# Kernel tuning notes

Hardware: AMD Instinct MI355X
Metric: run time of the kernel (lower is better)

Reference implementation:

```python
import jax, jax.numpy as jnp
import numpy as np

E = 8           # num_local_experts
H = 1024        # hidden_size
F = 1024        # moe_ffn_hidden_size (per-half; fc1 out = 2*F due to GLU)
T = 16384       # total dispatched tokens
GLU_LINEAR_OFFSET = 1.0


def setup_inputs() -> dict:
    key = jax.random.key(0)
    ks = jax.random.split(key, 7)
    s1 = 1.0 / np.sqrt(H)
    s2 = 1.0 / np.sqrt(F)
    return {
        "hidden_states": jax.random.normal(ks[0], (T, H), jnp.float32),
        "tokens_per_expert": jnp.full((E,), T // E, dtype=jnp.int64),
        "probs": jax.random.uniform(ks[1], (T,), jnp.float32),
        # expert params; torch Linear W is [out,in], stored here as [in,out] (same math)
        "W1": jax.random.uniform(ks[2], (E, H, 2 * F), jnp.float32, -s1, s1),
        "b1": jax.random.uniform(ks[3], (E, 2 * F), jnp.float32, -s1, s1),
        "W2": jax.random.uniform(ks[4], (E, F, H), jnp.float32, -s2, s2),
        "b2": jax.random.uniform(ks[5], (E, H), jnp.float32, -s2, s2),
    }


def reference(hidden_states, tokens_per_expert, probs, W1, b1, W2, b2):
    # Tokens arrive grouped contiguously by expert with equal counts (as in
    # setup_inputs), so the split/loop/cat in the torch module is exactly a
    # reshape + grouped (batched) GEMM over the expert axis.
    e = W1.shape[0]
    t, h = hidden_states.shape
    x = hidden_states.reshape(e, t // e, h)            # [E, Tpe, H]
    p = probs.reshape(e, t // e)                       # [E, Tpe]
    # fc1 (gated)
    y = jnp.einsum('eth,ehf->etf', x, W1) + b1[:, None, :]  # [E, Tpe, 2F]
    gate, lin = jnp.split(y, 2, axis=-1)
    a = jax.nn.silu(gate) * (lin + GLU_LINEAR_OFFSET)       # [E, Tpe, F]
    a = a * p[..., None]                                    # per-token scale
    # fc2
    out = jnp.einsum('etf,efh->eth', a, W2) + b2[:, None, :]
    return out.reshape(t, h)
```

## Files before the change

### kernel.cpp

```cpp
#include <hip/hip_runtime.h>
#include <hip/hip_bf16.h>
#include <stdint.h>

#define T_TOK 16384
#define H_DIM 1024
#define F_DIM 1024
#define E_NUM 8
#define TPE   2048

typedef unsigned short u16;
typedef __attribute__((ext_vector_type(8))) short bf16x8;
typedef __attribute__((ext_vector_type(4))) float f32x4;
typedef __attribute__((ext_vector_type(8))) u16 u16x8;

__device__ __forceinline__ u16 f2bf(float x) {
  unsigned int u = __float_as_uint(x);
  u = (u + 0x7fffu + ((u >> 16) & 1u)) >> 16;
  return (u16)u;
}

#define GLD16(gp, lp)                                                          \
  __builtin_amdgcn_global_load_lds(                                            \
      (const __attribute__((address_space(1))) void*)(gp),                     \
      (__attribute__((address_space(3))) void*)(lp), 16, 0, 0)

__global__ __launch_bounds__(256) void prep(
    const float* __restrict__ x, const float* __restrict__ W1,
    const float* __restrict__ W2, u16* __restrict__ xbf,
    u16* __restrict__ w1t, u16* __restrict__ w2t) {
  __shared__ float tile[64][65];
  const int b = blockIdx.x;
  const int t = threadIdx.x;
  if (b < 2048) {
    const int n8 = (T_TOK * H_DIM) / 8;
    for (int i = b * 256 + t; i < n8; i += 2048 * 256) {
      const float4* s = (const float4*)(x + (size_t)i * 8);
      float4 a = s[0], c = s[1];
      u16x8 o;
      o[0] = f2bf(a.x); o[1] = f2bf(a.y); o[2] = f2bf(a.z); o[3] = f2bf(a.w);
      o[4] = f2bf(c.x); o[5] = f2bf(c.y); o[6] = f2bf(c.z); o[7] = f2bf(c.w);
      *(u16x8*)(xbf + (size_t)i * 8) = o;
    }
    return;
  }
  const float* src; u16* dst; int R, C, id;
  if (b < 6144) { src = W1; dst = w1t; R = H_DIM; C = 2 * F_DIM; id = b - 2048; }
  else          { src = W2; dst = w2t; R = F_DIM; C = H_DIM;     id = b - 6144; }
  int nCt = C >> 6, nRt = R >> 6;
  int per = nCt * nRt;
  int e = id / per;
  int r2 = id - e * per;
  int rt = r2 / nCt, ct = r2 - rt * nCt;
  const float* s = src + (size_t)e * R * C + (size_t)(rt << 6) * C + (ct << 6);
  int lr = t >> 4, lc = (t & 15) << 2;
#pragma unroll
  for (int i = 0; i < 4; i++) {
    float4 v = *(const float4*)(s + (size_t)(lr + i * 16) * C + lc);
    tile[lr + i * 16][lc + 0] = v.x;
    tile[lr + i * 16][lc + 1] = v.y;
    tile[lr + i * 16][lc + 2] = v.z;
    tile[lr + i * 16][lc + 3] = v.w;
  }
  __syncthreads();
  u16* d = dst + (size_t)e * C * R + (size_t)(ct << 6) * R + (rt << 6);
  int orow = t >> 2, ok = (t & 3) << 4;
  u16x8 o0, o1;
#pragma unroll
  for (int i = 0; i < 8; i++) o0[i] = f2bf(tile[ok + i][orow]);
#pragma unroll
  for (int i = 0; i < 8; i++) o1[i] = f2bf(tile[ok + 8 + i][orow]);
  *(u16x8*)(d + (size_t)orow * R + ok) = o0;
  *(u16x8*)(d + (size_t)orow * R + ok + 8) = o1;
}


#define DSA(b, mi)                                                             \
  _Pragma("unroll") for (int m2_ = 0; m2_ < 2; ++m2_)                          \
  _Pragma("unroll") for (int ks_ = 0; ks_ < 2; ++ks_)                          \
      aF[m2_][ks_] = *(const bf16x8*)(sm + (b) * 32768 + aRowBase +            \
                                      ((mi) * 2 + m2_) * 2048 + koff[ks_]);

#define DSB(b)                                                                 \
  _Pragma("unroll") for (int n_ = 0; n_ < 4; ++n_)                             \
  _Pragma("unroll") for (int ks_ = 0; ks_ < 2; ++ks_)                          \
      bF[n_][ks_] = *(const bf16x8*)(sm + 65536 + (b) * 32768 + bRowBase +     \
                                     n_ * 2048 + koff[ks_]);

#define MFMA16(mi)                                                             \
  _Pragma("unroll") for (int n_ = 0; n_ < 4; ++n_)                             \
  _Pragma("unroll") for (int m2_ = 0; m2_ < 2; ++m2_)                          \
  _Pragma("unroll") for (int ks_ = 0; ks_ < 2; ++ks_)                          \
      acc[(mi) * 2 + m2_][n_] = __builtin_amdgcn_mfma_f32_16x16x32_bf16(       \
          aF[m2_][ks_], bF[n_][ks_], acc[(mi) * 2 + m2_][n_], 0, 0, 0);

#define PF_A(db, q, d) GLD16(aP[q] + (d), sm + (db) * 32768 + (q) * 8192 + tid * 16)
#define PF_B(db, q, d) GLD16(bP[q] + (d), sm + 65536 + (db) * 32768 + (q) * 8192 + tid * 16)

#define PHASE(b, mi, PFC, WTC)                                                 \
  do {                                                                         \
    DSA(b, mi);                                                                \
    if ((mi) == 0) { DSB(b); }                                                 \
    PFC                                                                        \
    __builtin_amdgcn_s_setprio(1);                                             \
    MFMA16(mi);                                                                \
    __builtin_amdgcn_s_setprio(0);                                             \
    WTC                                                                        \
    __builtin_amdgcn_s_barrier();                                              \
  } while (0)

#define KLOOP_BODY                                                             \
         \
  PF_B(0, 0, 0); PF_B(0, 1, 0); PF_B(0, 2, 0); PF_B(0, 3, 0);                  \
  PF_A(0, 0, 0); PF_A(0, 1, 0); PF_A(0, 2, 0); PF_A(0, 3, 0);                  \
  PF_B(1, 0, 64); PF_B(1, 1, 64); PF_B(1, 2, 64); PF_B(1, 3, 64);              \
  asm volatile("s_waitcnt vmcnt(4)" ::: "memory");                             \
  __builtin_amdgcn_s_barrier();                                                \
  for (int it = 0; it < 7; ++it) {                                             \
    PHASE(0, 0, PF_A(1, 0, 64); PF_A(1, 1, 64);, );                            \
    PHASE(0, 1, PF_A(1, 2, 64); PF_A(1, 3, 64);, );                            \
    PHASE(0, 2, PF_B(0, 0, 128); PF_B(0, 1, 128);, );                          \
    PHASE(0, 3, PF_B(0, 2, 128); PF_B(0, 3, 128);,                             \
          asm volatile("s_waitcnt vmcnt(4)" ::: "memory"););                   \
    PHASE(1, 0, PF_A(0, 0, 128); PF_A(0, 1, 128);, );                          \
    PHASE(1, 1, PF_A(0, 2, 128); PF_A(0, 3, 128);, );                          \
    PHASE(1, 2, PF_B(1, 0, 192); PF_B(1, 1, 192);, );                          \
    PHASE(1, 3, PF_B(1, 2, 192); PF_B(1, 3, 192);,                             \
          asm volatile("s_waitcnt vmcnt(4)" ::: "memory"););                   \
    _Pragma("unroll") for (int q_ = 0; q_ < 4; ++q_) {                         \
      aP[q_] += 128; bP[q_] += 128;                                            \
    }                                                                          \
  }                                                                            \
                   \
  PHASE(0, 0, PF_A(1, 0, 64); PF_A(1, 1, 64);, );                              \
  PHASE(0, 1, PF_A(1, 2, 64); PF_A(1, 3, 64);, );                              \
  PHASE(0, 2, , );                                                             \
  PHASE(0, 3, , asm volatile("s_waitcnt vmcnt(0)" ::: "memory"););             \
  PHASE(1, 0, , );                                                             \
  PHASE(1, 1, , );                                                             \
  PHASE(1, 2, , );                                                             \
  PHASE(1, 3, , );

__global__ __launch_bounds__(512, 2) void gemm1_8p(
    const u16* __restrict__ xbf, const u16* __restrict__ w1t,
    const float* __restrict__ b1, const float* __restrict__ probs,
    u16* __restrict__ abf) {
  extern __shared__ char sm[];
  const int tid = threadIdx.x;
  const int lane = tid & 63;
  const int wid = tid >> 6;
  const int wm = wid >> 2, wn = wid & 3;
  const int bid = blockIdx.x;
  const int e = bid & 7;
  const int inner = bid >> 3;
  const int mt = inner >> 3, ct = inner & 7;
  const int tokBase = e * TPE + mt * 256;
  const int c0 = ct * 128;
  const int lrow = lane & 15, lkhi = lane >> 4;

  const u16* aP[4]; const u16* bP[4];
#pragma unroll
  for (int q = 0; q < 4; ++q) {
    int lin = q * 8192 + tid * 16;
    int lg = lin ^ (((lin >> 7) & 7) << 4);
    int row = lg >> 7, kk = (lg & 127) >> 1;
    aP[q] = xbf + (size_t)(tokBase + row) * H_DIM + kk;
    int col = (((row >> 5) & 1) << 10) + c0 + ((row >> 6) << 5) + (row & 31);
    bP[q] = w1t + (size_t)(e * 2 * F_DIM + col) * H_DIM + kk;
  }
  const int aRowBase = (wm * 128 + lrow) * 128;
  const int bRowBase = (wn * 64 + lrow) * 128;
  int koff[2];
#pragma unroll
  for (int ks = 0; ks < 2; ++ks)
    koff[ks] = ((ks << 6) | (lkhi << 4)) ^ ((lane & 7) << 4);

  f32x4 acc[8][4];
#pragma unroll
  for (int i = 0; i < 8; ++i)
#pragma unroll
    for (int j = 0; j < 4; ++j) acc[i][j] = f32x4{0.f, 0.f, 0.f, 0.f};
  bf16x8 aF[2][2], bF[4][2];

  KLOOP_BODY

#pragma unroll
  for (int j = 0; j < 2; ++j) {
    int cf = c0 + wn * 32 + j * 16 + lrow;
    float gb = b1[e * 2 * F_DIM + cf];
    float lb = b1[e * 2 * F_DIM + F_DIM + cf];
#pragma unroll
    for (int i = 0; i < 8; ++i) {
      int trow = tokBase + wm * 128 + i * 16 + lkhi * 4;
#pragma unroll
      for (int r = 0; r < 4; ++r) {
        float g = acc[i][j][r] + gb;
        float l = acc[i][j + 2][r] + lb + 1.0f;
        float p = probs[trow + r];
        float sig = 1.0f / (1.0f + __expf(-g));
        abf[(size_t)(trow + r) * F_DIM + cf] = f2bf(g * sig * l * p);
      }
    }
  }
}

__global__ __launch_bounds__(512, 2) void gemm2_8p(
    const u16* __restrict__ abf, const u16* __restrict__ w2t,
    const float* __restrict__ b2, float* __restrict__ out) {
  extern __shared__ char sm[];
  const int tid = threadIdx.x;
  const int lane = tid & 63;
  const int wid = tid >> 6;
  const int wm = wid >> 2, wn = wid & 3;
  const int bid = blockIdx.x;
  const int e = bid & 7;
  const int inner = bid >> 3;
  const int mt = inner >> 2, nt = inner & 3;
  const int tokBase = e * TPE + mt * 256;
  const int h0 = nt * 256;
  const int lrow = lane & 15, lkhi = lane >> 4;

  const u16* aP[4]; const u16* bP[4];
#pragma unroll
  for (int q = 0; q < 4; ++q) {
    int lin = q * 8192 + tid * 16;
    int lg = lin ^ (((lin >> 7) & 7) << 4);
    int row = lg >> 7, kk = (lg & 127) >> 1;
    aP[q] = abf + (size_t)(tokBase + row) * F_DIM + kk;
    bP[q] = w2t + (size_t)(e * H_DIM + h0 + row) * F_DIM + kk;
  }
  const int aRowBase = (wm * 128 + lrow) * 128;
  const int bRowBase = (wn * 64 + lrow) * 128;
  int koff[2];
#pragma unroll
  for (int ks = 0; ks < 2; ++ks)
    koff[ks] = ((ks << 6) | (lkhi << 4)) ^ ((lane & 7) << 4);

  f32x4 acc[8][4];
#pragma unroll
  for (int i = 0; i < 8; ++i)
#pragma unroll
    for (int j = 0; j < 4; ++j) acc[i][j] = f32x4{0.f, 0.f, 0.f, 0.f};
  bf16x8 aF[2][2], bF[4][2];

  KLOOP_BODY

#pragma unroll
  for (int j = 0; j < 4; ++j) {
    int h = h0 + wn * 64 + j * 16 + lrow;
    float bb = b2[e * H_DIM + h];
#pragma unroll
    for (int i = 0; i < 8; ++i) {
      int trow = tokBase + wm * 128 + i * 16 + lkhi * 4;
#pragma unroll
      for (int r = 0; r < 4; ++r)
        out[(size_t)(trow + r) * H_DIM + h] = acc[i][j][r] + bb;
    }
  }
}

extern "C" void kernel_launch(void* const* d_in, const int* in_sizes, int n_in,
                              void* d_out, int out_size, void* d_ws,
                              size_t ws_size, hipStream_t stream) {
  const float* x     = (const float*)d_in[0];
  const float* probs = (const float*)d_in[2];
  const float* W1    = (const float*)d_in[3];
  const float* b1    = (const float*)d_in[4];
  const float* W2    = (const float*)d_in[5];
  const float* b2    = (const float*)d_in[6];
  float* out = (float*)d_out;

  if (ws_size < 117440512u) return;
  char* ws = (char*)d_ws;
  u16* xbf = (u16*)(ws);
  u16* w1t = (u16*)(ws + 33554432);
  u16* w2t = (u16*)(ws + 67108864);
  u16* abf = (u16*)(ws + 83886080);

  (void)hipFuncSetAttribute(reinterpret_cast<const void*>(gemm1_8p),
                            hipFuncAttributeMaxDynamicSharedMemorySize, 131072);
  (void)hipFuncSetAttribute(reinterpret_cast<const void*>(gemm2_8p),
                            hipFuncAttributeMaxDynamicSharedMemorySize, 131072);

  prep<<<8192, 256, 0, stream>>>(x, W1, W2, xbf, w1t, w2t);
  gemm1_8p<<<E_NUM * 8 * 8, 512, 131072, stream>>>(xbf, w1t, b1, probs, abf);
  gemm2_8p<<<E_NUM * 8 * 4, 512, 131072, stream>>>(abf, w2t, b2, out);
}
```

Measured before the change: 151.5 us.

## Fuse fp32-to-bf16 activation conversion into gemm1 A-tile loading

Removes the separate pass that converts the fp32 hidden states to a bf16 workspace buffer. Gemm1 now loads fp32 A tiles into registers, converts them and writes them to LDS inside the pipelined K loop, while the weight transpose becomes two standalone kernels. This avoids writing and re-reading a 32MB intermediate, but doubles the A-operand global traffic per tile (re-read across the 8 column tiles), adds VGPR pressure and conversion ALU work in the hot loop, and changes the wait-count pipelining.

Result: slower. 169.6 us (+12.0%).

```diff
diff --git a/kernel.cpp b/kernel.cpp
--- a/kernel.cpp
+++ b/kernel.cpp
@@ -24,34 +24,17 @@
       (const __attribute__((address_space(1))) void*)(gp),                     \
       (__attribute__((address_space(3))) void*)(lp), 16, 0, 0)
 
-__global__ __launch_bounds__(256) void prep(
-    const float* __restrict__ x, const float* __restrict__ W1,
-    const float* __restrict__ W2, u16* __restrict__ xbf,
-    u16* __restrict__ w1t, u16* __restrict__ w2t) {
+__global__ __launch_bounds__(256) void transpose_cvt(
+    const float* __restrict__ src, u16* __restrict__ dst, int R, int C) {
   __shared__ float tile[64][65];
-  const int b = blockIdx.x;
-  const int t = threadIdx.x;
-  if (b < 2048) {
-    const int n8 = (T_TOK * H_DIM) / 8;
-    for (int i = b * 256 + t; i < n8; i += 2048 * 256) {
-      const float4* s = (const float4*)(x + (size_t)i * 8);
-      float4 a = s[0], c = s[1];
-      u16x8 o;
-      o[0] = f2bf(a.x); o[1] = f2bf(a.y); o[2] = f2bf(a.z); o[3] = f2bf(a.w);
-      o[4] = f2bf(c.x); o[5] = f2bf(c.y); o[6] = f2bf(c.z); o[7] = f2bf(c.w);
-      *(u16x8*)(xbf + (size_t)i * 8) = o;
-    }
-    return;
-  }
-  const float* src; u16* dst; int R, C, id;
-  if (b < 6144) { src = W1; dst = w1t; R = H_DIM; C = 2 * F_DIM; id = b - 2048; }
-  else          { src = W2; dst = w2t; R = F_DIM; C = H_DIM;     id = b - 6144; }
   int nCt = C >> 6, nRt = R >> 6;
   int per = nCt * nRt;
-  int e = id / per;
-  int r2 = id - e * per;
+  int b = blockIdx.x;
+  int e = b / per;
+  int r2 = b - e * per;
   int rt = r2 / nCt, ct = r2 - rt * nCt;
   const float* s = src + (size_t)e * R * C + (size_t)(rt << 6) * C + (ct << 6);
+  int t = threadIdx.x;
   int lr = t >> 4, lc = (t & 15) << 2;
 #pragma unroll
   for (int i = 0; i < 4; i++) {
@@ -96,8 +79,35 @@
 #define PF_A(db, q, d) GLD16(aP[q] + (d), sm + (db) * 32768 + (q) * 8192 + tid * 16)
 #define PF_B(db, q, d) GLD16(bP[q] + (d), sm + 65536 + (db) * 32768 + (q) * 8192 + tid * 16)
 
-#define PHASE(b, mi, PFC, WTC)                                                 \
+#define VMW(N) asm volatile("s_waitcnt vmcnt(" #N ")" ::: "memory");
+
+#define A_WAIT(N)                                                              \
+  asm volatile("s_waitcnt vmcnt(" #N ")" ::: "memory");                        \
+  __builtin_amdgcn_sched_barrier(0);
+
+#define A_ISSUE(OFFE)                                                          \
+  _Pragma("unroll") for (int q_ = 0; q_ < 4; ++q_) {                           \
+    const float* p_ = afp[q_] + (OFFE);                                        \
+    asm volatile("global_load_dwordx4 %0, %2, off\n\t"                         \
+                 "global_load_dwordx4 %1, %2, off offset:16"                   \
+                 : "=&v"(av[2 * q_]), "=&v"(av[2 * q_ + 1])                    \
+                 : "v"(p_));                                                   \
+  }
+
+#define A_CVTWRITE(db)                                                         \
+  _Pragma("unroll") for (int q_ = 0; q_ < 4; ++q_) {                           \
+    u16x8 w_;                                                                  \
+    _Pragma("unroll") for (int e_ = 0; e_ < 4; ++e_) {                         \
+      w_[e_] = f2bf(av[2 * q_][e_]);                                           \
+      w_[e_ + 4] = f2bf(av[2 * q_ + 1][e_]);                                   \
+    }                                                                          \
+    *(u16x8*)(sm + (db) * 32768 + q_ * 8192 + tid * 16) = w_;                  \
+  }                                                                            \
+  __builtin_amdgcn_sched_barrier(0);
+
+#define PHASE1(b, mi, PRE, PFC, WTC)                                           \
   do {                                                                         \
+    PRE                                                                        \
     DSA(b, mi);                                                                \
     if ((mi) == 0) { DSB(b); }                                                 \
     PFC                                                                        \
@@ -108,40 +118,8 @@
     __builtin_amdgcn_s_barrier();                                              \
   } while (0)
 
-#define KLOOP_BODY                                                             \
-         \
-  PF_B(0, 0, 0); PF_B(0, 1, 0); PF_B(0, 2, 0); PF_B(0, 3, 0);                  \
-  PF_A(0, 0, 0); PF_A(0, 1, 0); PF_A(0, 2, 0); PF_A(0, 3, 0);                  \
-  PF_B(1, 0, 64); PF_B(1, 1, 64); PF_B(1, 2, 64); PF_B(1, 3, 64);              \
-  asm volatile("s_waitcnt vmcnt(4)" ::: "memory");                             \
-  __builtin_amdgcn_s_barrier();                                                \
-  for (int it = 0; it < 7; ++it) {                                             \
-    PHASE(0, 0, PF_A(1, 0, 64); PF_A(1, 1, 64);, );                            \
-    PHASE(0, 1, PF_A(1, 2, 64); PF_A(1, 3, 64);, );                            \
-    PHASE(0, 2, PF_B(0, 0, 128); PF_B(0, 1, 128);, );                          \
-    PHASE(0, 3, PF_B(0, 2, 128); PF_B(0, 3, 128);,                             \
-          asm volatile("s_waitcnt vmcnt(4)" ::: "memory"););                   \
-    PHASE(1, 0, PF_A(0, 0, 128); PF_A(0, 1, 128);, );                          \
-    PHASE(1, 1, PF_A(0, 2, 128); PF_A(0, 3, 128);, );                          \
-    PHASE(1, 2, PF_B(1, 0, 192); PF_B(1, 1, 192);, );                          \
-    PHASE(1, 3, PF_B(1, 2, 192); PF_B(1, 3, 192);,                             \
-          asm volatile("s_waitcnt vmcnt(4)" ::: "memory"););                   \
-    _Pragma("unroll") for (int q_ = 0; q_ < 4; ++q_) {                         \
-      aP[q_] += 128; bP[q_] += 128;                                            \
-    }                                                                          \
-  }                                                                            \
-                   \
-  PHASE(0, 0, PF_A(1, 0, 64); PF_A(1, 1, 64);, );                              \
-  PHASE(0, 1, PF_A(1, 2, 64); PF_A(1, 3, 64);, );                              \
-  PHASE(0, 2, , );                                                             \
-  PHASE(0, 3, , asm volatile("s_waitcnt vmcnt(0)" ::: "memory"););             \
-  PHASE(1, 0, , );                                                             \
-  PHASE(1, 1, , );                                                             \
-  PHASE(1, 2, , );                                                             \
-  PHASE(1, 3, , );
-
 __global__ __launch_bounds__(512, 2) void gemm1_8p(
-    const u16* __restrict__ xbf, const u16* __restrict__ w1t,
+    const float* __restrict__ x, const u16* __restrict__ w1t,
     const float* __restrict__ b1, const float* __restrict__ probs,
     u16* __restrict__ abf) {
   extern __shared__ char sm[];
@@ -157,13 +135,14 @@
   const int c0 = ct * 128;
   const int lrow = lane & 15, lkhi = lane >> 4;
 
-  const u16* aP[4]; const u16* bP[4];
+  const float* afp[4];
+  const u16* bP[4];
 #pragma unroll
   for (int q = 0; q < 4; ++q) {
     int lin = q * 8192 + tid * 16;
     int lg = lin ^ (((lin >> 7) & 7) << 4);
     int row = lg >> 7, kk = (lg & 127) >> 1;
-    aP[q] = xbf + (size_t)(tokBase + row) * H_DIM + kk;
+    afp[q] = x + (size_t)(tokBase + row) * H_DIM + kk;
     int col = (((row >> 5) & 1) << 10) + c0 + ((row >> 6) << 5) + (row & 31);
     bP[q] = w1t + (size_t)(e * 2 * F_DIM + col) * H_DIM + kk;
   }
@@ -180,8 +159,37 @@
 #pragma unroll
     for (int j = 0; j < 4; ++j) acc[i][j] = f32x4{0.f, 0.f, 0.f, 0.f};
   bf16x8 aF[2][2], bF[4][2];
-
-  KLOOP_BODY
+  float4 av[8];
+
+  A_ISSUE(0);
+  PF_B(0, 0, 0); PF_B(0, 1, 0); PF_B(0, 2, 0); PF_B(0, 3, 0);
+  A_WAIT(4); A_CVTWRITE(0);
+  A_ISSUE(64);
+  PF_B(1, 0, 64); PF_B(1, 1, 64); PF_B(1, 2, 64); PF_B(1, 3, 64);
+  VMW(12)
+  asm volatile("s_waitcnt lgkmcnt(0)" ::: "memory");
+  __builtin_amdgcn_s_barrier();
+
+  for (int it = 0; it < 7; ++it) {
+    PHASE1(0, 0, A_WAIT(4) A_CVTWRITE(1) A_ISSUE(128), , );
+    PHASE1(0, 1, , , );
+    PHASE1(0, 2, , PF_B(0, 0, 128); PF_B(0, 1, 128);, );
+    PHASE1(0, 3, , PF_B(0, 2, 128); PF_B(0, 3, 128);, VMW(12));
+    PHASE1(1, 0, A_WAIT(4) A_CVTWRITE(0) A_ISSUE(192), , );
+    PHASE1(1, 1, , , );
+    PHASE1(1, 2, , PF_B(1, 0, 192); PF_B(1, 1, 192);, );
+    PHASE1(1, 3, , PF_B(1, 2, 192); PF_B(1, 3, 192);, VMW(12));
+#pragma unroll
+    for (int q_ = 0; q_ < 4; ++q_) { afp[q_] += 128; bP[q_] += 128; }
+  }
+  PHASE1(0, 0, A_WAIT(4) A_CVTWRITE(1), , );
+  PHASE1(0, 1, , , );
+  PHASE1(0, 2, , , );
+  PHASE1(0, 3, , , VMW(0));
+  PHASE1(1, 0, , , );
+  PHASE1(1, 1, , , );
+  PHASE1(1, 2, , , );
+  PHASE1(1, 3, , , );
 
 #pragma unroll
   for (int j = 0; j < 2; ++j) {
@@ -202,6 +210,18 @@
     }
   }
 }
+
+#define PHASE2(b, mi, PFC, WTC)                                                \
+  do {                                                                         \
+    DSA(b, mi);                                                                \
+    if ((mi) == 0) { DSB(b); }                                                 \
+    PFC                                                                        \
+    __builtin_amdgcn_s_setprio(1);                                             \
+    MFMA16(mi);                                                                \
+    __builtin_amdgcn_s_setprio(0);                                             \
+    WTC                                                                        \
+    __builtin_amdgcn_s_barrier();                                              \
+  } while (0)
 
 __global__ __launch_bounds__(512, 2) void gemm2_8p(
     const u16* __restrict__ abf, const u16* __restrict__ w2t,
@@ -242,7 +262,31 @@
     for (int j = 0; j < 4; ++j) acc[i][j] = f32x4{0.f, 0.f, 0.f, 0.f};
   bf16x8 aF[2][2], bF[4][2];
 
-  KLOOP_BODY
+  PF_B(0, 0, 0); PF_B(0, 1, 0); PF_B(0, 2, 0); PF_B(0, 3, 0);
+  PF_A(0, 0, 0); PF_A(0, 1, 0); PF_A(0, 2, 0); PF_A(0, 3, 0);
+  PF_B(1, 0, 64); PF_B(1, 1, 64); PF_B(1, 2, 64); PF_B(1, 3, 64);
+  VMW(4)
+  __builtin_amdgcn_s_barrier();
+  for (int it = 0; it < 7; ++it) {
+    PHASE2(0, 0, PF_A(1, 0, 64); PF_A(1, 1, 64);, );
+    PHASE2(0, 1, PF_A(1, 2, 64); PF_A(1, 3, 64);, );
+    PHASE2(0, 2, PF_B(0, 0, 128); PF_B(0, 1, 128);, );
+    PHASE2(0, 3, PF_B(0, 2, 128); PF_B(0, 3, 128);, VMW(4));
+    PHASE2(1, 0, PF_A(0, 0, 128); PF_A(0, 1, 128);, );
+    PHASE2(1, 1, PF_A(0, 2, 128); PF_A(0, 3, 128);, );
+    PHASE2(1, 2, PF_B(1, 0, 192); PF_B(1, 1, 192);, );
+    PHASE2(1, 3, PF_B(1, 2, 192); PF_B(1, 3, 192);, VMW(4));
+#pragma unroll
+    for (int q_ = 0; q_ < 4; ++q_) { aP[q_] += 128; bP[q_] += 128; }
+  }
+  PHASE2(0, 0, PF_A(1, 0, 64); PF_A(1, 1, 64);, );
+  PHASE2(0, 1, PF_A(1, 2, 64); PF_A(1, 3, 64);, );
+  PHASE2(0, 2, , );
+  PHASE2(0, 3, , VMW(0));
+  PHASE2(1, 0, , );
+  PHASE2(1, 1, , );
+  PHASE2(1, 2, , );
+  PHASE2(1, 3, , );
 
 #pragma unroll
   for (int j = 0; j < 4; ++j) {
@@ -269,19 +313,21 @@
   const float* b2    = (const float*)d_in[6];
   float* out = (float*)d_out;
 
-  if (ws_size < 117440512u) return;
+  if (ws_size < 83886080u) return;
   char* ws = (char*)d_ws;
-  u16* xbf = (u16*)(ws);
-  u16* w1t = (u16*)(ws + 33554432);
-  u16* w2t = (u16*)(ws + 67108864);
-  u16* abf = (u16*)(ws + 83886080);
+  u16* w1t = (u16*)(ws);
+  u16* w2t = (u16*)(ws + 33554432);
+  u16* abf = (u16*)(ws + 50331648);
 
   (void)hipFuncSetAttribute(reinterpret_cast<const void*>(gemm1_8p),
                             hipFuncAttributeMaxDynamicSharedMemorySize, 131072);
   (void)hipFuncSetAttribute(reinterpret_cast<const void*>(gemm2_8p),
                             hipFuncAttributeMaxDynamicSharedMemorySize, 131072);
 
-  prep<<<8192, 256, 0, stream>>>(x, W1, W2, xbf, w1t, w2t);
-  gemm1_8p<<<E_NUM * 8 * 8, 512, 131072, stream>>>(xbf, w1t, b1, probs, abf);
+  transpose_cvt<<<E_NUM * (2 * F_DIM / 64) * (H_DIM / 64), 256, 0, stream>>>(
+      W1, w1t, H_DIM, 2 * F_DIM);
+  transpose_cvt<<<E_NUM * (H_DIM / 64) * (F_DIM / 64), 256, 0, stream>>>(
+      W2, w2t, F_DIM, H_DIM);
+  gemm1_8p<<<E_NUM * 8 * 8, 512, 131072, stream>>>(x, w1t, b1, probs, abf);
   gemm2_8p<<<E_NUM * 8 * 4, 512, 131072, stream>>>(abf, w2t, b2, out);
 }
```
